# Performance work log

Hardware: AMD Instinct MI355X
Metric: run time of the kernel (lower is better)

The kernel has to match this reference:

```python
import jax, jax.numpy as jnp
import numpy as np

NUM_USERS = 100_000
NUM_ITEMS = 50_000
N = NUM_USERS + NUM_ITEMS
E_DIR = 600_000            # directed user->item interactions
E = 2 * E_DIR              # bidirectional edge list used by LGConv
D = 64                     # embed_dim
F_EDGE = 8                 # edge_mlp_input_dim (edge_attr 7 + edge_weight_init 1)
H_MLP = 32                 # edge_mlp_hidden_dim
NUM_ARTISTS = 20_000
NUM_ALBUMS = 40_000
NUM_LAYERS = 3
AUDIO_SCALE = 0.3
META_SCALE = 0.44


def l2norm(x, eps=1e-12):
    # matches torch F.normalize(p=2, dim=-1)
    n = jnp.linalg.norm(x, axis=-1, keepdims=True)
    return x / jnp.maximum(n, eps)


def setup_inputs() -> dict:
    key = jax.random.key(0)
    ks = jax.random.split(key, 12)
    u = jax.random.randint(ks[0], (E_DIR,), 0, NUM_USERS)
    it = jax.random.randint(ks[1], (E_DIR,), 0, NUM_ITEMS) + NUM_USERS
    # bidirectional edges over the concatenated [user; item] node space
    edge_index = jnp.stack([jnp.concatenate([u, it]), jnp.concatenate([it, u])], axis=0)
    return {
        'user_emb_w': 0.01 * jax.random.normal(ks[2], (NUM_USERS, D), jnp.float32),
        'item_audio_emb': jax.random.normal(ks[3], (NUM_ITEMS, D), jnp.float32),
        'artist_emb_w': jax.random.normal(ks[4], (NUM_ARTISTS, D), jnp.float32) * (6.0 / (NUM_ARTISTS + D)) ** 0.5,
        'album_emb_w': jax.random.normal(ks[5], (NUM_ALBUMS, D), jnp.float32) * (6.0 / (NUM_ALBUMS + D)) ** 0.5,
        'mlp_w1': jax.random.normal(ks[6], (F_EDGE, H_MLP), jnp.float32) * (1.0 / F_EDGE) ** 0.5,
        'mlp_b1': jnp.zeros((H_MLP,), jnp.float32),
        'mlp_w2': jax.random.normal(ks[7], (H_MLP, 1), jnp.float32) * (1.0 / H_MLP) ** 0.5,
        'mlp_b2': jnp.zeros((1,), jnp.float32),
        'edge_features': jax.random.uniform(ks[8], (E, F_EDGE), jnp.float32),
        'edge_index': edge_index,
        'artist_ids': jax.random.randint(ks[9], (NUM_ITEMS,), 0, NUM_ARTISTS),
        'album_ids': jax.random.randint(ks[10], (NUM_ITEMS,), 0, NUM_ALBUMS),
    }


def reference(user_emb_w, item_audio_emb, artist_emb_w, album_emb_w,
              mlp_w1, mlp_b1, mlp_w2, mlp_b2, edge_features,
              edge_index, artist_ids, album_ids):
    # Edge weight MLP: Linear -> ReLU -> Linear -> Sigmoid -> squeeze
    h = jax.nn.relu(edge_features @ mlp_w1 + mlp_b1)
    edge_w = jax.nn.sigmoid(h @ mlp_w2 + mlp_b2)[:, 0]  # [E]

    # Node features
    user = l2norm(user_emb_w)
    meta = artist_emb_w[artist_ids] + album_emb_w[album_ids]
    item = l2norm(item_audio_emb * AUDIO_SCALE + meta * META_SCALE)
    x = jnp.concatenate([user, item], axis=0)  # [N, D]

    row, col = edge_index[0], edge_index[1]

    # gcn_norm (add_self_loops=False): deg over destination column
    deg = jax.ops.segment_sum(edge_w, col, num_segments=N)
    dinv = jnp.where(deg > 0, 1.0 / jnp.sqrt(jnp.where(deg > 0, deg, 1.0)), 0.0)
    norm = dinv[row] * edge_w * dinv[col]  # [E]

    acc = x
    for _ in range(NUM_LAYERS):
        msg = norm[:, None] * x[row]                         # gather [E, D]
        x = jax.ops.segment_sum(msg, col, num_segments=N)    # scatter-add
        acc = acc + x
    x = l2norm(acc / (NUM_LAYERS + 1))

    user_emb = x[:NUM_USERS]
    item_emb = x[NUM_USERS:]
    align_loss = jnp.float32(0.0)
    return user_emb, item_emb, align_loss
```

## Files before the change

kernel.cpp:

```cpp
#include <hip/hip_runtime.h>
#include <math.h>

#define NUM_USERS 100000
#define NUM_ITEMS 50000
#define NN 150000
#define EE 1200000
#define NNP 150016
#define G8_BLOCKS 4688

#define NBUCKET 293
#define NB2 256
#define EPB 4688

typedef unsigned short ushort_t;
typedef unsigned int uint_t;

__device__ __forceinline__ uint_t pack2(float lo, float hi) {
    uint_t a = __float_as_uint(lo);
    uint_t b = __float_as_uint(hi);
    a = (a + 0x7FFFu + ((a >> 16) & 1u)) >> 16;
    b = (b + 0x7FFFu + ((b >> 16) & 1u)) & 0xFFFF0000u;
    return a | b;
}
__device__ __forceinline__ float lo16(uint_t x) { return __uint_as_float(x << 16); }
__device__ __forceinline__ float hi16(uint_t x) { return __uint_as_float(x & 0xFFFF0000u); }

__global__ void mlp_kernel(const float* __restrict__ feats,
                           const float* __restrict__ w1,
                           const float* __restrict__ b1,
                           const float* __restrict__ w2,
                           const float* __restrict__ b2,
                           float* __restrict__ wout) {
    __shared__ float sw1t[256];
    __shared__ float2 shb[32];
    __shared__ float sb2s;
    int t = threadIdx.x;
    sw1t[t] = w1[(t & 7) * 32 + (t >> 3)];
    if (t < 32) shb[t] = make_float2(b1[t], w2[t]);
    if (t == 0) sb2s = b2[0];
    __syncthreads();
    int e = blockIdx.x * 256 + t;
    if (e >= EE) return;
    const float4* fp = (const float4*)(feats + (size_t)e * 8);
    float4 fa = fp[0], fb = fp[1];
    float f[8] = {fa.x, fa.y, fa.z, fa.w, fb.x, fb.y, fb.z, fb.w};
    float s = sb2s;
#pragma unroll
    for (int j = 0; j < 32; ++j) {
        float4 wa = *(const float4*)&sw1t[j * 8];
        float4 wb = *(const float4*)&sw1t[j * 8 + 4];
        float2 bw = shb[j];
        float h = bw.x;
        h = fmaf(f[0], wa.x, h);
        h = fmaf(f[1], wa.y, h);
        h = fmaf(f[2], wa.z, h);
        h = fmaf(f[3], wa.w, h);
        h = fmaf(f[4], wb.x, h);
        h = fmaf(f[5], wb.y, h);
        h = fmaf(f[6], wb.z, h);
        h = fmaf(f[7], wb.w, h);
        h = fmaxf(h, 0.f);
        s = fmaf(h, bw.y, s);
    }
    wout[e] = 1.f / (1.f + expf(-s));
}

__global__ void hist_kernel(const int* __restrict__ col,
                            int* __restrict__ hist) {
    __shared__ int h[NBUCKET];
    int t = threadIdx.x, B = blockIdx.x;
    for (int i = t; i < NBUCKET; i += 256) h[i] = 0;
    __syncthreads();
    int beg = B * EPB, end = beg + EPB; if (end > EE) end = EE;
    for (int i = beg + t; i < end; i += 256)
        atomicAdd(&h[col[i] >> 9], 1);
    __syncthreads();
    for (int i = t; i < NBUCKET; i += 256) hist[i * NB2 + B] = h[i];
}

__global__ void scanb_kernel(int* __restrict__ hist,
                             int* __restrict__ tot) {
    int b = blockIdx.x, t = threadIdx.x;
    int v = hist[b * NB2 + t];
    int lane = t & 63;
    int s = v;
#pragma unroll
    for (int off = 1; off < 64; off <<= 1) {
        int u = __shfl_up(s, off, 64);
        if (lane >= off) s += u;
    }
    __shared__ int wsum[4];
    if (lane == 63) wsum[t >> 6] = s;
    __syncthreads();
    int add = 0;
    for (int w = 0; w < (t >> 6); ++w) add += wsum[w];
    hist[b * NB2 + t] = s - v + add;
    if (t == 255) tot[b] = s + add;
}

__global__ void scant_kernel(const int* __restrict__ tot,
                             int* __restrict__ base) {
    int t = threadIdx.x;
    int v = (t < NBUCKET) ? tot[t] : 0;
    int lane = t & 63;
    int s = v;
#pragma unroll
    for (int off = 1; off < 64; off <<= 1) {
        int u = __shfl_up(s, off, 64);
        if (lane >= off) s += u;
    }
    __shared__ int wsum[8];
    if (lane == 63) wsum[t >> 6] = s;
    __syncthreads();
    int add = 0;
    for (int w = 0; w < (t >> 6); ++w) add += wsum[w];
    if (t < NBUCKET) base[t] = s - v + add;
    if (t == 511) base[NBUCKET] = s + add;
}

__global__ void scatter1_kernel(const int* __restrict__ col,
                                const int* __restrict__ row,
                                const float* __restrict__ wbuf,
                                const int* __restrict__ hist,
                                const int* __restrict__ base,
                                int2* __restrict__ tmp) {
    __shared__ int bbase[NBUCKET];
    __shared__ int cur[NBUCKET];
    int t = threadIdx.x, B = blockIdx.x;
    for (int i = t; i < NBUCKET; i += 256) {
        bbase[i] = base[i] + hist[i * NB2 + B];
        cur[i] = 0;
    }
    __syncthreads();
    int beg = B * EPB, end = beg + EPB; if (end > EE) end = EE;
    for (int i = beg + t; i < end; i += 256) {
        int c = col[i];
        int b = c >> 9;
        int r = atomicAdd(&cur[b], 1);
        tmp[bbase[b] + r] = make_int2((row[i] << 9) | (c & 511),
                                      __float_as_int(wbuf[i]));
    }
}

__global__ void scatter2_kernel(const int2* __restrict__ tmp,
                                const int* __restrict__ base,
                                int* __restrict__ offs,
                                int2* __restrict__ packed,
                                float* __restrict__ dinv) {
    __shared__ int sc[512];
    __shared__ float sdeg[512];
    __shared__ int wsum[8];
    int b = blockIdx.x, t = threadIdx.x;
    int beg = base[b], end = base[b + 1];
    sc[t] = 0;
    sdeg[t] = 0.f;
    __syncthreads();
    for (int i = beg + t; i < end; i += 512) {
        int2 rec = tmp[i];
        int cl = rec.x & 511;
        atomicAdd(&sc[cl], 1);
        atomicAdd(&sdeg[cl], __int_as_float(rec.y));
    }
    __syncthreads();
    int v = sc[t];
    int lane = t & 63;
    int s = v;
#pragma unroll
    for (int off = 1; off < 64; off <<= 1) {
        int u = __shfl_up(s, off, 64);
        if (lane >= off) s += u;
    }
    if (lane == 63) wsum[t >> 6] = s;
    __syncthreads();
    int add = 0;
    for (int w = 0; w < (t >> 6); ++w) add += wsum[w];
    int excl = s - v + add;
    offs[b * 512 + t] = beg + excl;
    int g = b * 512 + t;
    if (g < NN) {
        float ds = sdeg[t];
        dinv[g] = (ds > 0.f) ? rsqrtf(ds) : 0.f;
    }
    __syncthreads();
    sc[t] = excl;
    __syncthreads();
    for (int i = beg + t; i < end; i += 512) {
        int2 rec = tmp[i];
        int r = atomicAdd(&sc[rec.x & 511], 1);
        packed[beg + r] = make_int2(((uint_t)rec.x) >> 9, rec.y);
    }
}

__device__ __forceinline__ void gather_node8(const ushort_t* __restrict__ zin,
                                             const int2* __restrict__ packed,
                                             int beg, int end, unsigned c,
                                             float4& a0, float4& a1) {
    for (int base = beg; base < end; base += 8) {
        int m = end - base; if (m > 8) m = 8;
        int r = 0; float w = 0.f;
        if ((int)c < m) {
            int2 p = packed[base + (int)c];
            r = p.x; w = __int_as_float(p.y);
        }
        int rj[8]; float wj[8]; uint4 vj[8];
#pragma unroll
        for (int u = 0; u < 8; ++u) {
            int idx = (u < m) ? u : (m - 1);
            rj[u] = __shfl(r, idx, 8);
            wj[u] = __shfl(w, u, 8);
        }
#pragma unroll
        for (int u = 0; u < 8; ++u)
            vj[u] = *(const uint4*)(zin + (size_t)(uint_t)rj[u] * 64u + c * 8u);
#pragma unroll
        for (int u = 0; u < 8; ++u) {
            float ww = wj[u]; uint4 v = vj[u];
            a0.x = fmaf(ww, lo16(v.x), a0.x);
            a0.y = fmaf(ww, hi16(v.x), a0.y);
            a0.z = fmaf(ww, lo16(v.y), a0.z);
            a0.w = fmaf(ww, hi16(v.y), a0.w);
            a1.x = fmaf(ww, lo16(v.z), a1.x);
            a1.y = fmaf(ww, hi16(v.z), a1.y);
            a1.z = fmaf(ww, lo16(v.w), a1.z);
            a1.w = fmaf(ww, hi16(v.w), a1.w);
        }
    }
}

__global__ void dinv_init_kernel(const int* __restrict__ offs,
                                 const float* __restrict__ user_w,
                                 const float* __restrict__ audio,
                                 const float* __restrict__ artist_w,
                                 const float* __restrict__ album_w,
                                 const int* __restrict__ artist_ids,
                                 const int* __restrict__ album_ids,
                                 const float* __restrict__ dinv,
                                 ushort_t* __restrict__ z0) {
    unsigned t = blockIdx.x * 256u + threadIdx.x;
    unsigned node = t >> 3, c = t & 7u;
    if (node >= NN) return;
    float d = dinv[node];

    size_t ri = (size_t)node * 64u + c * 8u;
    float v[8];
    if (node < NUM_USERS) {
        float4 x0 = *(const float4*)(user_w + ri);
        float4 x1 = *(const float4*)(user_w + ri + 4);
        v[0]=x0.x; v[1]=x0.y; v[2]=x0.z; v[3]=x0.w;
        v[4]=x1.x; v[5]=x1.y; v[6]=x1.z; v[7]=x1.w;
    } else {
        unsigned j = node - NUM_USERS;
        unsigned aid = (unsigned)artist_ids[j], bid = (unsigned)album_ids[j];
        const float* ap = artist_w + (size_t)aid * 64u + c * 8u;
        const float* bp = album_w  + (size_t)bid * 64u + c * 8u;
        const float* up = audio    + (size_t)j   * 64u + c * 8u;
        float4 A0 = *(const float4*)ap, A1 = *(const float4*)(ap + 4);
        float4 B0 = *(const float4*)bp, B1 = *(const float4*)(bp + 4);
        float4 U0 = *(const float4*)up, U1 = *(const float4*)(up + 4);
        v[0] = fmaf(0.44f, A0.x + B0.x, 0.3f * U0.x);
        v[1] = fmaf(0.44f, A0.y + B0.y, 0.3f * U0.y);
        v[2] = fmaf(0.44f, A0.z + B0.z, 0.3f * U0.z);
        v[3] = fmaf(0.44f, A0.w + B0.w, 0.3f * U0.w);
        v[4] = fmaf(0.44f, A1.x + B1.x, 0.3f * U1.x);
        v[5] = fmaf(0.44f, A1.y + B1.y, 0.3f * U1.y);
        v[6] = fmaf(0.44f, A1.z + B1.z, 0.3f * U1.z);
        v[7] = fmaf(0.44f, A1.w + B1.w, 0.3f * U1.w);
    }
    float s = 0.f;
#pragma unroll
    for (int k = 0; k < 8; ++k) s = fmaf(v[k], v[k], s);
    s += __shfl_xor(s, 1, 8);
    s += __shfl_xor(s, 2, 8);
    s += __shfl_xor(s, 4, 8);
    float rn = rsqrtf(fmaxf(s, 1e-24f));
    float scale = ((d > 0.f) ? d : 1.f) * rn;
    uint4 o;
    o.x = pack2(v[0] * scale, v[1] * scale);
    o.y = pack2(v[2] * scale, v[3] * scale);
    o.z = pack2(v[4] * scale, v[5] * scale);
    o.w = pack2(v[6] * scale, v[7] * scale);
    *(uint4*)(z0 + ri) = o;
}

__global__ void spmm_kernel(const ushort_t* __restrict__ zin,
                            const int2* __restrict__ packed,
                            const int* __restrict__ offs,
                            const float* __restrict__ dinv,
                            ushort_t* __restrict__ zout) {
    unsigned t = blockIdx.x * 256u + threadIdx.x;
    unsigned node = t >> 3, c = t & 7u;
    if (node >= NN) return;
    float4 a0 = make_float4(0,0,0,0), a1 = make_float4(0,0,0,0);
    gather_node8(zin, packed, offs[node], offs[node + 1], c, a0, a1);
    float d = dinv[node], dd = d * d;
    uint4 o;
    o.x = pack2(a0.x * dd, a0.y * dd);
    o.y = pack2(a0.z * dd, a0.w * dd);
    o.z = pack2(a1.x * dd, a1.y * dd);
    o.w = pack2(a1.z * dd, a1.w * dd);
    *(uint4*)(zout + (size_t)node * 64u + c * 8u) = o;
}

__global__ void spmm_final_kernel(const ushort_t* __restrict__ z0,
                                  const ushort_t* __restrict__ z1,
                                  const ushort_t* __restrict__ z2,
                                  const int2* __restrict__ packed,
                                  const int* __restrict__ offs,
                                  const float* __restrict__ dinv,
                                  float* __restrict__ out) {
    unsigned t = blockIdx.x * 256u + threadIdx.x;
    unsigned node = t >> 3, c = t & 7u;
    if (node >= NN) return;
    float4 a0 = make_float4(0,0,0,0), a1 = make_float4(0,0,0,0);
    gather_node8(z2, packed, offs[node], offs[node + 1], c, a0, a1);
    float d = dinv[node], dd = d * d;
    size_t ri = (size_t)node * 64u + c * 8u;
    uint4 p0 = *(const uint4*)(z0 + ri);
    uint4 p1 = *(const uint4*)(z1 + ri);
    uint4 p2 = *(const uint4*)(z2 + ri);
    float v[8];
    v[0] = lo16(p0.x) + lo16(p1.x) + lo16(p2.x) + a0.x * dd;
    v[1] = hi16(p0.x) + hi16(p1.x) + hi16(p2.x) + a0.y * dd;
    v[2] = lo16(p0.y) + lo16(p1.y) + lo16(p2.y) + a0.z * dd;
    v[3] = hi16(p0.y) + hi16(p1.y) + hi16(p2.y) + a0.w * dd;
    v[4] = lo16(p0.z) + lo16(p1.z) + lo16(p2.z) + a1.x * dd;
    v[5] = hi16(p0.z) + hi16(p1.z) + hi16(p2.z) + a1.y * dd;
    v[6] = lo16(p0.w) + lo16(p1.w) + lo16(p2.w) + a1.z * dd;
    v[7] = hi16(p0.w) + hi16(p1.w) + hi16(p2.w) + a1.w * dd;
    float s = 0.f;
#pragma unroll
    for (int k = 0; k < 8; ++k) s = fmaf(v[k], v[k], s);
    s += __shfl_xor(s, 1, 8);
    s += __shfl_xor(s, 2, 8);
    s += __shfl_xor(s, 4, 8);
    float n = fmaxf(sqrtf(s) * 0.25f, 1e-12f);
    float inv = 0.25f / n;
    float4 o0 = make_float4(v[0]*inv, v[1]*inv, v[2]*inv, v[3]*inv);
    float4 o1 = make_float4(v[4]*inv, v[5]*inv, v[6]*inv, v[7]*inv);
    *(float4*)(out + ri)     = o0;
    *(float4*)(out + ri + 4) = o1;
    if (t == 0) out[(size_t)NN * 64u] = 0.f;
}

extern "C" void kernel_launch(void* const* d_in, const int* in_sizes, int n_in,
                              void* d_out, int out_size, void* d_ws, size_t ws_size,
                              hipStream_t stream) {
    const float* user_w     = (const float*)d_in[0];
    const float* audio      = (const float*)d_in[1];
    const float* artist_w   = (const float*)d_in[2];
    const float* album_w    = (const float*)d_in[3];
    const float* w1         = (const float*)d_in[4];
    const float* b1         = (const float*)d_in[5];
    const float* w2         = (const float*)d_in[6];
    const float* b2         = (const float*)d_in[7];
    const float* feats      = (const float*)d_in[8];
    const int*   row        = (const int*)d_in[9];
    const int*   col        = row + EE;
    const int*   artist_ids = (const int*)d_in[10];
    const int*   album_ids  = (const int*)d_in[11];
    float* out = (float*)d_out;

    int*      hist    = (int*)d_ws;
    int*      tot     = hist + NBUCKET * NB2;
    int*      base    = tot + 512;
    int*      offs    = base + 512;
    float*    wbuf    = (float*)(offs + NNP + 16);
    float*    dinv    = wbuf + EE;
    int2*     packed  = (int2*)(dinv + NN);
    ushort_t* z0      = (ushort_t*)(packed + EE);
    ushort_t* z1      = z0 + (size_t)NN * 64;
    ushort_t* z2      = z1 + (size_t)NN * 64;
    int2*     tmp     = (int2*)z1;

    mlp_kernel<<<(EE + 255) / 256, 256, 0, stream>>>(feats, w1, b1, w2, b2, wbuf);
    hist_kernel<<<NB2, 256, 0, stream>>>(col, hist);
    scanb_kernel<<<NBUCKET, 256, 0, stream>>>(hist, tot);
    scant_kernel<<<1, 512, 0, stream>>>(tot, base);
    scatter1_kernel<<<NB2, 256, 0, stream>>>(col, row, wbuf, hist, base, tmp);
    scatter2_kernel<<<NBUCKET, 512, 0, stream>>>(tmp, base, offs, packed, dinv);
    dinv_init_kernel<<<G8_BLOCKS, 256, 0, stream>>>(offs,
                                                    user_w, audio, artist_w, album_w,
                                                    artist_ids, album_ids, dinv, z0);
    spmm_kernel<<<G8_BLOCKS, 256, 0, stream>>>(z0, packed, offs, dinv, z1);
    spmm_kernel<<<G8_BLOCKS, 256, 0, stream>>>(z1, packed, offs, dinv, z2);
    spmm_final_kernel<<<G8_BLOCKS, 256, 0, stream>>>(z0, z1, z2, packed, offs,
                                                     dinv, out);
}
```

Before: 302.3 us.

## Fuse scan kernels via last-block pattern and fold node init into scatter2

Merges the per-bucket scan and the total scan into one kernel. The last block to finish, detected with an atomic counter reset in hist_kernel, computes the bucket bases. It also removes the separate dinv_init kernel by computing the normalized, dinv-scaled bf16 initial embeddings inside scatter2 from the shared degree array. This cuts two kernel launches and a global re-read of dinv, at the cost of more serial work per scatter2 block (293 blocks covering 150k nodes) and lower parallelism for the init phase.

```diff
diff --git a/kernel.cpp b/kernel.cpp
--- a/kernel.cpp
+++ b/kernel.cpp
@@ -66,9 +66,11 @@
 }
 
 __global__ void hist_kernel(const int* __restrict__ col,
-                            int* __restrict__ hist) {
+                            int* __restrict__ hist,
+                            int* __restrict__ done) {
     __shared__ int h[NBUCKET];
     int t = threadIdx.x, B = blockIdx.x;
+    if (B == 0 && t == 0) *done = 0;
     for (int i = t; i < NBUCKET; i += 256) h[i] = 0;
     __syncthreads();
     int beg = B * EPB, end = beg + EPB; if (end > EE) end = EE;
@@ -78,44 +80,45 @@
     for (int i = t; i < NBUCKET; i += 256) hist[i * NB2 + B] = h[i];
 }
 
-__global__ void scanb_kernel(int* __restrict__ hist,
-                             int* __restrict__ tot) {
+__global__ void scanbt_kernel(int* __restrict__ hist,
+                              int* __restrict__ tot,
+                              int* __restrict__ base,
+                              int* __restrict__ done) {
+    __shared__ int wsum[8];
+    __shared__ int lastflag;
     int b = blockIdx.x, t = threadIdx.x;
-    int v = hist[b * NB2 + t];
     int lane = t & 63;
+    int v = (t < NB2) ? hist[b * NB2 + t] : 0;
     int s = v;
 #pragma unroll
     for (int off = 1; off < 64; off <<= 1) {
         int u = __shfl_up(s, off, 64);
         if (lane >= off) s += u;
     }
-    __shared__ int wsum[4];
     if (lane == 63) wsum[t >> 6] = s;
     __syncthreads();
     int add = 0;
-    for (int w = 0; w < (t >> 6); ++w) add += wsum[w];
-    hist[b * NB2 + t] = s - v + add;
-    if (t == 255) tot[b] = s + add;
-}
-
-__global__ void scant_kernel(const int* __restrict__ tot,
-                             int* __restrict__ base) {
-    int t = threadIdx.x;
-    int v = (t < NBUCKET) ? tot[t] : 0;
-    int lane = t & 63;
-    int s = v;
-#pragma unroll
-    for (int off = 1; off < 64; off <<= 1) {
-        int u = __shfl_up(s, off, 64);
-        if (lane >= off) s += u;
-    }
-    __shared__ int wsum[8];
-    if (lane == 63) wsum[t >> 6] = s;
-    __syncthreads();
-    int add = 0;
-    for (int w = 0; w < (t >> 6); ++w) add += wsum[w];
-    if (t < NBUCKET) base[t] = s - v + add;
-    if (t == 511) base[NBUCKET] = s + add;
+    for (int w = 0; w < (t >> 6) && w < 4; ++w) add += wsum[w];
+    if (t < NB2) hist[b * NB2 + t] = s - v + add;
+    if (t == NB2 - 1) atomicExch(&tot[b], s + add);
+    __syncthreads();
+    if (t == 0) lastflag = (atomicAdd(done, 1) == NBUCKET - 1);
+    __syncthreads();
+    if (lastflag) {
+        int v2 = (t < NBUCKET) ? atomicOr(&tot[t], 0) : 0;
+        int s2 = v2;
+#pragma unroll
+        for (int off = 1; off < 64; off <<= 1) {
+            int u = __shfl_up(s2, off, 64);
+            if (lane >= off) s2 += u;
+        }
+        if (lane == 63) wsum[t >> 6] = s2;
+        __syncthreads();
+        int add2 = 0;
+        for (int w = 0; w < (t >> 6); ++w) add2 += wsum[w];
+        if (t < NBUCKET) base[t] = s2 - v2 + add2;
+        if (t == 511) base[NBUCKET] = s2 + add2;
+    }
 }
 
 __global__ void scatter1_kernel(const int* __restrict__ col,
@@ -146,7 +149,14 @@
                                 const int* __restrict__ base,
                                 int* __restrict__ offs,
                                 int2* __restrict__ packed,
-                                float* __restrict__ dinv) {
+                                float* __restrict__ dinv,
+                                const float* __restrict__ user_w,
+                                const float* __restrict__ audio,
+                                const float* __restrict__ artist_w,
+                                const float* __restrict__ album_w,
+                                const int* __restrict__ artist_ids,
+                                const int* __restrict__ album_ids,
+                                ushort_t* __restrict__ z0) {
     __shared__ int sc[512];
     __shared__ float sdeg[512];
     __shared__ int wsum[8];
@@ -188,6 +198,54 @@
         int2 rec = tmp[i];
         int r = atomicAdd(&sc[rec.x & 511], 1);
         packed[beg + r] = make_int2(((uint_t)rec.x) >> 9, rec.y);
+    }
+    unsigned c = t & 7u;
+#pragma unroll
+    for (int sweep = 0; sweep < 8; ++sweep) {
+        int ln = sweep * 64 + (t >> 3);
+        unsigned node = (unsigned)b * 512u + ln;
+        if (node >= NN) continue;
+        float ds = sdeg[ln];
+        float d = (ds > 0.f) ? rsqrtf(ds) : 0.f;
+        size_t ri = (size_t)node * 64u + c * 8u;
+        float vv[8];
+        if (node < NUM_USERS) {
+            float4 x0 = *(const float4*)(user_w + ri);
+            float4 x1 = *(const float4*)(user_w + ri + 4);
+            vv[0]=x0.x; vv[1]=x0.y; vv[2]=x0.z; vv[3]=x0.w;
+            vv[4]=x1.x; vv[5]=x1.y; vv[6]=x1.z; vv[7]=x1.w;
+        } else {
+            unsigned j = node - NUM_USERS;
+            unsigned aid = (unsigned)artist_ids[j], bid = (unsigned)album_ids[j];
+            const float* ap = artist_w + (size_t)aid * 64u + c * 8u;
+            const float* bp = album_w  + (size_t)bid * 64u + c * 8u;
+            const float* up = audio    + (size_t)j   * 64u + c * 8u;
+            float4 A0 = *(const float4*)ap, A1 = *(const float4*)(ap + 4);
+            float4 B0 = *(const float4*)bp, B1 = *(const float4*)(bp + 4);
+            float4 U0 = *(const float4*)up, U1 = *(const float4*)(up + 4);
+            vv[0] = fmaf(0.44f, A0.x + B0.x, 0.3f * U0.x);
+            vv[1] = fmaf(0.44f, A0.y + B0.y, 0.3f * U0.y);
+            vv[2] = fmaf(0.44f, A0.z + B0.z, 0.3f * U0.z);
+            vv[3] = fmaf(0.44f, A0.w + B0.w, 0.3f * U0.w);
+            vv[4] = fmaf(0.44f, A1.x + B1.x, 0.3f * U1.x);
+            vv[5] = fmaf(0.44f, A1.y + B1.y, 0.3f * U1.y);
+            vv[6] = fmaf(0.44f, A1.z + B1.z, 0.3f * U1.z);
+            vv[7] = fmaf(0.44f, A1.w + B1.w, 0.3f * U1.w);
+        }
+        float ss = 0.f;
+#pragma unroll
+        for (int k = 0; k < 8; ++k) ss = fmaf(vv[k], vv[k], ss);
+        ss += __shfl_xor(ss, 1, 8);
+        ss += __shfl_xor(ss, 2, 8);
+        ss += __shfl_xor(ss, 4, 8);
+        float rn = rsqrtf(fmaxf(ss, 1e-24f));
+        float scale = ((d > 0.f) ? d : 1.f) * rn;
+        uint4 o;
+        o.x = pack2(vv[0] * scale, vv[1] * scale);
+        o.y = pack2(vv[2] * scale, vv[3] * scale);
+        o.z = pack2(vv[4] * scale, vv[5] * scale);
+        o.w = pack2(vv[6] * scale, vv[7] * scale);
+        *(uint4*)(z0 + ri) = o;
     }
 }
 
@@ -225,61 +283,6 @@
             a1.w = fmaf(ww, hi16(v.w), a1.w);
         }
     }
-}
-
-__global__ void dinv_init_kernel(const int* __restrict__ offs,
-                                 const float* __restrict__ user_w,
-                                 const float* __restrict__ audio,
-                                 const float* __restrict__ artist_w,
-                                 const float* __restrict__ album_w,
-                                 const int* __restrict__ artist_ids,
-                                 const int* __restrict__ album_ids,
-                                 const float* __restrict__ dinv,
-                                 ushort_t* __restrict__ z0) {
-    unsigned t = blockIdx.x * 256u + threadIdx.x;
-    unsigned node = t >> 3, c = t & 7u;
-    if (node >= NN) return;
-    float d = dinv[node];
-
-    size_t ri = (size_t)node * 64u + c * 8u;
-    float v[8];
-    if (node < NUM_USERS) {
-        float4 x0 = *(const float4*)(user_w + ri);
-        float4 x1 = *(const float4*)(user_w + ri + 4);
-        v[0]=x0.x; v[1]=x0.y; v[2]=x0.z; v[3]=x0.w;
-        v[4]=x1.x; v[5]=x1.y; v[6]=x1.z; v[7]=x1.w;
-    } else {
-        unsigned j = node - NUM_USERS;
-        unsigned aid = (unsigned)artist_ids[j], bid = (unsigned)album_ids[j];
-        const float* ap = artist_w + (size_t)aid * 64u + c * 8u;
-        const float* bp = album_w  + (size_t)bid * 64u + c * 8u;
-        const float* up = audio    + (size_t)j   * 64u + c * 8u;
-        float4 A0 = *(const float4*)ap, A1 = *(const float4*)(ap + 4);
-        float4 B0 = *(const float4*)bp, B1 = *(const float4*)(bp + 4);
-        float4 U0 = *(const float4*)up, U1 = *(const float4*)(up + 4);
-        v[0] = fmaf(0.44f, A0.x + B0.x, 0.3f * U0.x);
-        v[1] = fmaf(0.44f, A0.y + B0.y, 0.3f * U0.y);
-        v[2] = fmaf(0.44f, A0.z + B0.z, 0.3f * U0.z);
-        v[3] = fmaf(0.44f, A0.w + B0.w, 0.3f * U0.w);
-        v[4] = fmaf(0.44f, A1.x + B1.x, 0.3f * U1.x);
-        v[5] = fmaf(0.44f, A1.y + B1.y, 0.3f * U1.y);
-        v[6] = fmaf(0.44f, A1.z + B1.z, 0.3f * U1.z);
-        v[7] = fmaf(0.44f, A1.w + B1.w, 0.3f * U1.w);
-    }
-    float s = 0.f;
-#pragma unroll
-    for (int k = 0; k < 8; ++k) s = fmaf(v[k], v[k], s);
-    s += __shfl_xor(s, 1, 8);
-    s += __shfl_xor(s, 2, 8);
-    s += __shfl_xor(s, 4, 8);
-    float rn = rsqrtf(fmaxf(s, 1e-24f));
-    float scale = ((d > 0.f) ? d : 1.f) * rn;
-    uint4 o;
-    o.x = pack2(v[0] * scale, v[1] * scale);
-    o.y = pack2(v[2] * scale, v[3] * scale);
-    o.z = pack2(v[4] * scale, v[5] * scale);
-    o.w = pack2(v[6] * scale, v[7] * scale);
-    *(uint4*)(z0 + ri) = o;
 }
 
 __global__ void spmm_kernel(const ushort_t* __restrict__ zin,
@@ -363,7 +366,8 @@
     int*      hist    = (int*)d_ws;
     int*      tot     = hist + NBUCKET * NB2;
     int*      base    = tot + 512;
-    int*      offs    = base + 512;
+    int*      done    = base + 512;
+    int*      offs    = done + 16;
     float*    wbuf    = (float*)(offs + NNP + 16);
     float*    dinv    = wbuf + EE;
     int2*     packed  = (int2*)(dinv + NN);
@@ -373,14 +377,12 @@
     int2*     tmp     = (int2*)z1;
 
     mlp_kernel<<<(EE + 255) / 256, 256, 0, stream>>>(feats, w1, b1, w2, b2, wbuf);
-    hist_kernel<<<NB2, 256, 0, stream>>>(col, hist);
-    scanb_kernel<<<NBUCKET, 256, 0, stream>>>(hist, tot);
-    scant_kernel<<<1, 512, 0, stream>>>(tot, base);
+    hist_kernel<<<NB2, 256, 0, stream>>>(col, hist, done);
+    scanbt_kernel<<<NBUCKET, 512, 0, stream>>>(hist, tot, base, done);
     scatter1_kernel<<<NB2, 256, 0, stream>>>(col, row, wbuf, hist, base, tmp);
-    scatter2_kernel<<<NBUCKET, 512, 0, stream>>>(tmp, base, offs, packed, dinv);
-    dinv_init_kernel<<<G8_BLOCKS, 256, 0, stream>>>(offs,
-                                                    user_w, audio, artist_w, album_w,
-                                                    artist_ids, album_ids, dinv, z0);
+    scatter2_kernel<<<NBUCKET, 512, 0, stream>>>(tmp, base, offs, packed, dinv,
+                                                 user_w, audio, artist_w, album_w,
+                                                 artist_ids, album_ids, z0);
     spmm_kernel<<<G8_BLOCKS, 256, 0, stream>>>(z0, packed, offs, dinv, z1);
     spmm_kernel<<<G8_BLOCKS, 256, 0, stream>>>(z1, packed, offs, dinv, z2);
     spmm_final_kernel<<<G8_BLOCKS, 256, 0, stream>>>(z0, z1, z2, packed, offs,
```

New measurement: 346.1 us. 1.14x slower.

## Fuse scan kernels via last-block pattern and chain SpMM layers cooperatively

Applied to the files above, without the earlier changes.

Merges the two prefix-scan kernels into one, where the last block to finish (found through an atomic counter) scans the bucket totals. It also replaces the three SpMM launches with a single cooperative persistent kernel that uses grid-wide syncs between propagation layers. The aim is to cut kernel launch gaps and tail effects. In exchange, the grid is limited to the resident block count, which can lower memory-level parallelism, and grid.sync adds its own overhead; the old launches remain as a fallback if the cooperative launch fails.

```diff
diff --git a/kernel.cpp b/kernel.cpp
--- a/kernel.cpp
+++ b/kernel.cpp
@@ -1,5 +1,8 @@
 #include <hip/hip_runtime.h>
+#include <hip/hip_cooperative_groups.h>
 #include <math.h>
+
+namespace cg = cooperative_groups;
 
 #define NUM_USERS 100000
 #define NUM_ITEMS 50000
@@ -66,9 +69,11 @@
 }
 
 __global__ void hist_kernel(const int* __restrict__ col,
-                            int* __restrict__ hist) {
+                            int* __restrict__ hist,
+                            int* __restrict__ done) {
     __shared__ int h[NBUCKET];
     int t = threadIdx.x, B = blockIdx.x;
+    if (B == 0 && t == 0) *done = 0;
     for (int i = t; i < NBUCKET; i += 256) h[i] = 0;
     __syncthreads();
     int beg = B * EPB, end = beg + EPB; if (end > EE) end = EE;
@@ -78,44 +83,45 @@
     for (int i = t; i < NBUCKET; i += 256) hist[i * NB2 + B] = h[i];
 }
 
-__global__ void scanb_kernel(int* __restrict__ hist,
-                             int* __restrict__ tot) {
+__global__ void scanbt_kernel(int* __restrict__ hist,
+                              int* __restrict__ tot,
+                              int* __restrict__ base,
+                              int* __restrict__ done) {
+    __shared__ int wsum[8];
+    __shared__ int lastflag;
     int b = blockIdx.x, t = threadIdx.x;
-    int v = hist[b * NB2 + t];
     int lane = t & 63;
+    int v = (t < NB2) ? hist[b * NB2 + t] : 0;
     int s = v;
 #pragma unroll
     for (int off = 1; off < 64; off <<= 1) {
         int u = __shfl_up(s, off, 64);
         if (lane >= off) s += u;
     }
-    __shared__ int wsum[4];
     if (lane == 63) wsum[t >> 6] = s;
     __syncthreads();
     int add = 0;
-    for (int w = 0; w < (t >> 6); ++w) add += wsum[w];
-    hist[b * NB2 + t] = s - v + add;
-    if (t == 255) tot[b] = s + add;
-}
-
-__global__ void scant_kernel(const int* __restrict__ tot,
-                             int* __restrict__ base) {
-    int t = threadIdx.x;
-    int v = (t < NBUCKET) ? tot[t] : 0;
-    int lane = t & 63;
-    int s = v;
-#pragma unroll
-    for (int off = 1; off < 64; off <<= 1) {
-        int u = __shfl_up(s, off, 64);
-        if (lane >= off) s += u;
-    }
-    __shared__ int wsum[8];
-    if (lane == 63) wsum[t >> 6] = s;
-    __syncthreads();
-    int add = 0;
-    for (int w = 0; w < (t >> 6); ++w) add += wsum[w];
-    if (t < NBUCKET) base[t] = s - v + add;
-    if (t == 511) base[NBUCKET] = s + add;
+    for (int w = 0; w < (t >> 6) && w < 4; ++w) add += wsum[w];
+    if (t < NB2) hist[b * NB2 + t] = s - v + add;
+    if (t == NB2 - 1) atomicExch(&tot[b], s + add);
+    __syncthreads();
+    if (t == 0) lastflag = (atomicAdd(done, 1) == NBUCKET - 1);
+    __syncthreads();
+    if (lastflag) {
+        int v2 = (t < NBUCKET) ? atomicOr(&tot[t], 0) : 0;
+        int s2 = v2;
+#pragma unroll
+        for (int off = 1; off < 64; off <<= 1) {
+            int u = __shfl_up(s2, off, 64);
+            if (lane >= off) s2 += u;
+        }
+        if (lane == 63) wsum[t >> 6] = s2;
+        __syncthreads();
+        int add2 = 0;
+        for (int w = 0; w < (t >> 6); ++w) add2 += wsum[w];
+        if (t < NBUCKET) base[t] = s2 - v2 + add2;
+        if (t == 511) base[NBUCKET] = s2 + add2;
+    }
 }
 
 __global__ void scatter1_kernel(const int* __restrict__ col,
@@ -342,6 +348,85 @@
     if (t == 0) out[(size_t)NN * 64u] = 0.f;
 }
 
+__global__ void __launch_bounds__(256, 4)
+spmm_chain_kernel(const ushort_t* __restrict__ z0,
+                  const int2* __restrict__ packed,
+                  const int* __restrict__ offs,
+                  const float* __restrict__ dinv,
+                  ushort_t* __restrict__ z1,
+                  ushort_t* __restrict__ z2,
+                  float* __restrict__ out) {
+    cg::grid_group grid = cg::this_grid();
+    unsigned gtid = blockIdx.x * 256u + threadIdx.x;
+    unsigned stride = gridDim.x * 256u;
+    const unsigned NW = (unsigned)NN * 8u;
+
+    for (unsigned t = gtid; t < NW; t += stride) {
+        unsigned node = t >> 3, c = t & 7u;
+        float4 a0 = make_float4(0,0,0,0), a1 = make_float4(0,0,0,0);
+        gather_node8(z0, packed, offs[node], offs[node + 1], c, a0, a1);
+        float d = dinv[node], dd = d * d;
+        uint4 o;
+        o.x = pack2(a0.x * dd, a0.y * dd);
+        o.y = pack2(a0.z * dd, a0.w * dd);
+        o.z = pack2(a1.x * dd, a1.y * dd);
+        o.w = pack2(a1.z * dd, a1.w * dd);
+        *(uint4*)(z1 + (size_t)node * 64u + c * 8u) = o;
+    }
+    __threadfence();
+    grid.sync();
+    __threadfence();
+
+    for (unsigned t = gtid; t < NW; t += stride) {
+        unsigned node = t >> 3, c = t & 7u;
+        float4 a0 = make_float4(0,0,0,0), a1 = make_float4(0,0,0,0);
+        gather_node8(z1, packed, offs[node], offs[node + 1], c, a0, a1);
+        float d = dinv[node], dd = d * d;
+        uint4 o;
+        o.x = pack2(a0.x * dd, a0.y * dd);
+        o.y = pack2(a0.z * dd, a0.w * dd);
+        o.z = pack2(a1.x * dd, a1.y * dd);
+        o.w = pack2(a1.z * dd, a1.w * dd);
+        *(uint4*)(z2 + (size_t)node * 64u + c * 8u) = o;
+    }
+    __threadfence();
+    grid.sync();
+    __threadfence();
+
+    for (unsigned t = gtid; t < NW; t += stride) {
+        unsigned node = t >> 3, c = t & 7u;
+        float4 a0 = make_float4(0,0,0,0), a1 = make_float4(0,0,0,0);
+        gather_node8(z2, packed, offs[node], offs[node + 1], c, a0, a1);
+        float d = dinv[node], dd = d * d;
+        size_t ri = (size_t)node * 64u + c * 8u;
+        uint4 p0 = *(const uint4*)(z0 + ri);
+        uint4 p1 = *(const uint4*)(z1 + ri);
+        uint4 p2 = *(const uint4*)(z2 + ri);
+        float v[8];
+        v[0] = lo16(p0.x) + lo16(p1.x) + lo16(p2.x) + a0.x * dd;
+        v[1] = hi16(p0.x) + hi16(p1.x) + hi16(p2.x) + a0.y * dd;
+        v[2] = lo16(p0.y) + lo16(p1.y) + lo16(p2.y) + a0.z * dd;
+        v[3] = hi16(p0.y) + hi16(p1.y) + hi16(p2.y) + a0.w * dd;
+        v[4] = lo16(p0.z) + lo16(p1.z) + lo16(p2.z) + a1.x * dd;
+        v[5] = hi16(p0.z) + hi16(p1.z) + hi16(p2.z) + a1.y * dd;
+        v[6] = lo16(p0.w) + lo16(p1.w) + lo16(p2.w) + a1.z * dd;
+        v[7] = hi16(p0.w) + hi16(p1.w) + hi16(p2.w) + a1.w * dd;
+        float s = 0.f;
+#pragma unroll
+        for (int k = 0; k < 8; ++k) s = fmaf(v[k], v[k], s);
+        s += __shfl_xor(s, 1, 8);
+        s += __shfl_xor(s, 2, 8);
+        s += __shfl_xor(s, 4, 8);
+        float n = fmaxf(sqrtf(s) * 0.25f, 1e-12f);
+        float inv = 0.25f / n;
+        float4 o0 = make_float4(v[0]*inv, v[1]*inv, v[2]*inv, v[3]*inv);
+        float4 o1 = make_float4(v[4]*inv, v[5]*inv, v[6]*inv, v[7]*inv);
+        *(float4*)(out + ri)     = o0;
+        *(float4*)(out + ri + 4) = o1;
+    }
+    if (gtid == 0) out[(size_t)NN * 64u] = 0.f;
+}
+
 extern "C" void kernel_launch(void* const* d_in, const int* in_sizes, int n_in,
                               void* d_out, int out_size, void* d_ws, size_t ws_size,
                               hipStream_t stream) {
@@ -363,7 +448,8 @@
     int*      hist    = (int*)d_ws;
     int*      tot     = hist + NBUCKET * NB2;
     int*      base    = tot + 512;
-    int*      offs    = base + 512;
+    int*      done    = base + 512;
+    int*      offs    = done + 16;
     float*    wbuf    = (float*)(offs + NNP + 16);
     float*    dinv    = wbuf + EE;
     int2*     packed  = (int2*)(dinv + NN);
@@ -373,16 +459,42 @@
     int2*     tmp     = (int2*)z1;
 
     mlp_kernel<<<(EE + 255) / 256, 256, 0, stream>>>(feats, w1, b1, w2, b2, wbuf);
-    hist_kernel<<<NB2, 256, 0, stream>>>(col, hist);
-    scanb_kernel<<<NBUCKET, 256, 0, stream>>>(hist, tot);
-    scant_kernel<<<1, 512, 0, stream>>>(tot, base);
+    hist_kernel<<<NB2, 256, 0, stream>>>(col, hist, done);
+    scanbt_kernel<<<NBUCKET, 512, 0, stream>>>(hist, tot, base, done);
     scatter1_kernel<<<NB2, 256, 0, stream>>>(col, row, wbuf, hist, base, tmp);
     scatter2_kernel<<<NBUCKET, 512, 0, stream>>>(tmp, base, offs, packed, dinv);
     dinv_init_kernel<<<G8_BLOCKS, 256, 0, stream>>>(offs,
                                                     user_w, audio, artist_w, album_w,
                                                     artist_ids, album_ids, dinv, z0);
-    spmm_kernel<<<G8_BLOCKS, 256, 0, stream>>>(z0, packed, offs, dinv, z1);
-    spmm_kernel<<<G8_BLOCKS, 256, 0, stream>>>(z1, packed, offs, dinv, z2);
-    spmm_final_kernel<<<G8_BLOCKS, 256, 0, stream>>>(z0, z1, z2, packed, offs,
-                                                     dinv, out);
-}
+
+    static int chain_blocks = -1;
+    if (chain_blocks == -1) {
+        int per_cu = 0, num_cu = 0, dev = 0;
+        hipGetDevice(&dev);
+        hipDeviceGetAttribute(&num_cu, hipDeviceAttributeMultiprocessorCount, dev);
+        hipError_t oe = hipOccupancyMaxActiveBlocksPerMultiprocessor(
+            &per_cu, spmm_chain_kernel, 256, 0);
+        if (oe != hipSuccess || per_cu <= 0 || num_cu <= 0) chain_blocks = 0;
+        else {
+            long nb = (long)per_cu * num_cu;
+            if (nb > G8_BLOCKS) nb = G8_BLOCKS;
+            chain_blocks = (int)nb;
+        }
+    }
+    bool coop_done = false;
+    if (chain_blocks > 0) {
+        void* chain_args[] = {(void*)&z0, (void*)&packed, (void*)&offs,
+                              (void*)&dinv, (void*)&z1, (void*)&z2, (void*)&out};
+        hipError_t le = hipLaunchCooperativeKernel(spmm_chain_kernel,
+                                                   dim3(chain_blocks), dim3(256),
+                                                   chain_args, 0, stream);
+        if (le == hipSuccess) coop_done = true;
+        else chain_blocks = 0;
+    }
+    if (!coop_done) {
+        spmm_kernel<<<G8_BLOCKS, 256, 0, stream>>>(z0, packed, offs, dinv, z1);
+        spmm_kernel<<<G8_BLOCKS, 256, 0, stream>>>(z1, packed, offs, dinv, z2);
+        spmm_final_kernel<<<G8_BLOCKS, 256, 0, stream>>>(z0, z1, z2, packed, offs,
+                                                         dinv, out);
+    }
+}
```

New measurement: 808.4 us. 2.67x slower.
